# Optimization experiments

Hardware: AMD Instinct MI355X
Metric: run time of the kernel (lower is better)

Reference implementation:

```python
import jax, jax.numpy as jnp
import numpy as np

DIM = 384
NUM_HEADS = 6
HEAD_SIZE = DIM // NUM_HEADS


def setup_inputs() -> dict:
    key = jax.random.key(0)
    k1, k2, k3, k4, k5 = jax.random.split(key, 5)
    x = jax.random.normal(k1, (2, 4096, DIM), dtype=jnp.float32)
    # qkv Linear(dim, 3*dim): weight [3*dim, dim], bias [3*dim] (torch layout)
    w_qkv = jax.random.normal(k2, (3 * DIM, DIM), dtype=jnp.float32) * (1.0 / np.sqrt(DIM))
    b_qkv = jax.random.normal(k3, (3 * DIM,), dtype=jnp.float32) * 1e-6
    w_proj = jax.random.normal(k4, (DIM, DIM), dtype=jnp.float32) * (1.0 / np.sqrt(DIM))
    b_proj = jax.random.normal(k5, (DIM,), dtype=jnp.float32) * 0.01
    return {"x": x, "w_qkv": w_qkv, "b_qkv": b_qkv, "w_proj": w_proj, "b_proj": b_proj}


def reference(x, w_qkv, b_qkv, w_proj, b_proj):
    B, N, C = x.shape
    H, D = NUM_HEADS, HEAD_SIZE
    # qkv projection: [B, N, 3C]
    qkv = jnp.einsum("bnc,fc->bnf", x, w_qkv) + b_qkv
    # view(B, N, 3, H, D) -> permute to (3, B, H, N, D)
    qkv = qkv.reshape(B, N, 3, H, D).transpose(2, 0, 3, 1, 4)
    q, k, v = qkv[0], qkv[1], qkv[2]
    # full attention matrix [B, H, N, N] (matches the naive module)
    att = jnp.einsum("bhnd,bhmd->bhnm", q, k) / jnp.sqrt(jnp.float32(D)).astype(x.dtype)
    att = jax.nn.softmax(att, axis=-1)  # attn_drop p=0 -> identity
    out = jnp.einsum("bhnm,bhmd->bhnd", att, v)  # [B, H, N, D]
    out = out.transpose(0, 2, 1, 3).reshape(B, N, C)
    out = jnp.einsum("bnc,fc->bnf", out, w_proj) + b_proj  # proj_drop p=0 -> identity
    return out
```

## Files before the change

kernel.cpp:

```cpp
#include <hip/hip_runtime.h>
#include <stdint.h>

#define DIM   384
#define NH    6
#define SEQ   4096
#define MTOT  (2*SEQ)

typedef __bf16 bf16x8 __attribute__((ext_vector_type(8)));
typedef float  f32x4  __attribute__((ext_vector_type(4)));
typedef unsigned short u16;
typedef u16 u16x4 __attribute__((ext_vector_type(4)));
typedef u16 u16x8 __attribute__((ext_vector_type(8)));
typedef uint32_t u32x4 __attribute__((ext_vector_type(4)));

extern "C" __device__ float __ocml_native_exp2_f32(float);

__device__ __forceinline__ u16 f2b(float f) {
  uint32_t u = __builtin_bit_cast(uint32_t, f);
  u += 0x7fffu + ((u >> 16) & 1u);
  return (u16)(u >> 16);
}

#define GLDS16(gp, lp) \
  __builtin_amdgcn_global_load_lds((const __attribute__((address_space(1))) void*)(gp), \
                                   (__attribute__((address_space(3))) void*)(lp), 16, 0, 0)

__global__ void conv_bf16_kernel(const float* __restrict__ in, u16* __restrict__ out, int n8) {
  int i = blockIdx.x * 256 + threadIdx.x;
  if (i >= n8) return;
  float4 a = ((const float4*)in)[2*i];
  float4 b = ((const float4*)in)[2*i+1];
  u16x8 r;
  r[0]=f2b(a.x); r[1]=f2b(a.y); r[2]=f2b(a.z); r[3]=f2b(a.w);
  r[4]=f2b(b.x); r[5]=f2b(b.y); r[6]=f2b(b.z); r[7]=f2b(b.w);
  ((u16x8*)out)[i] = r;
}

template<int EPI>
__global__ __launch_bounds__(256) void gemm_bt_kernel(
    const u16* __restrict__ A,
    const u16* __restrict__ Bw,
    const float* __restrict__ bias,
    u16* __restrict__ Qb, u16* __restrict__ Kb, u16* __restrict__ Vt,
    float* __restrict__ Out)
{
  __shared__ u16 As[128*64];
  __shared__ u16 Bs[128*64];
  const int tid = threadIdx.x;
  const int wid = tid >> 6, lane = tid & 63;
  const int lr = lane & 15, lg = lane >> 4;
  const int m0 = blockIdx.x * 128;
  const int f0 = blockIdx.y * 128;
  const int wm = (wid >> 1) * 64, wn = (wid & 1) * 64;
  const f32x4 z4 = {0.f, 0.f, 0.f, 0.f};
  f32x4 acc[4][4];
  #pragma unroll
  for (int i = 0; i < 4; ++i)
    #pragma unroll
    for (int j = 0; j < 4; ++j) acc[i][j] = z4;

  for (int k0 = 0; k0 < 384; k0 += 64) {
    __syncthreads();
    #pragma unroll
    for (int i = 0; i < 4; ++i) {
      const int wb  = i*4096 + wid*1024;
      const int ob  = wb + lane*16;
      const int row = ob >> 7;
      const int lch = ((ob >> 4) & 7) ^ (row & 7);
      GLDS16(A  + (size_t)(m0+row)*384 + k0 + lch*8, As + wb/2);
      GLDS16(Bw + (size_t)(f0+row)*384 + k0 + lch*8, Bs + wb/2);
    }
    __syncthreads();
    #pragma unroll
    for (int ks = 0; ks < 2; ++ks) {
      bf16x8 af[4], bfr[4];
      #pragma unroll
      for (int mi = 0; mi < 4; ++mi) {
        int r = wm + mi*16 + lr;
        af[mi] = *(const bf16x8*)(As + (r*128 + ((ks*64 + lg*16) ^ ((r&7)<<4)))/2);
      }
      #pragma unroll
      for (int ni = 0; ni < 4; ++ni) {
        int r = wn + ni*16 + lr;
        bfr[ni] = *(const bf16x8*)(Bs + (r*128 + ((ks*64 + lg*16) ^ ((r&7)<<4)))/2);
      }
      #pragma unroll
      for (int mi = 0; mi < 4; ++mi)
        #pragma unroll
        for (int ni = 0; ni < 4; ++ni)
          acc[mi][ni] = __builtin_amdgcn_mfma_f32_16x16x32_bf16(af[mi], bfr[ni], acc[mi][ni], 0, 0, 0);
    }
  }

  if (EPI == 0) {
    const int which = f0 / 384;
    #pragma unroll
    for (int ni = 0; ni < 4; ++ni) {
      const int f   = f0 + wn + ni*16 + lr;
      const float bv = bias[f];
      const int rem = f - which*384;
      const int h = rem >> 6, d = rem & 63;
      #pragma unroll
      for (int mi = 0; mi < 4; ++mi) {
        const int m = m0 + wm + mi*16 + lg*4;
        const int b = m >> 12, n = m & 4095;
        const size_t bh = (size_t)(b*NH + h);
        if (which == 0) {
          #pragma unroll
          for (int j = 0; j < 4; ++j)
            Qb[(bh*SEQ + n + j)*64 + d] = f2b((acc[mi][ni][j] + bv) * 0.1803368801111244f);
        } else if (which == 1) {
          #pragma unroll
          for (int j = 0; j < 4; ++j)
            Kb[(bh*SEQ + n + j)*64 + d] = f2b(acc[mi][ni][j] + bv);
        } else {
          u16x4 pk;
          #pragma unroll
          for (int j = 0; j < 4; ++j) pk[j] = f2b(acc[mi][ni][j] + bv);
          *(u16x4*)(Vt + (bh*64 + d)*SEQ + n) = pk;
        }
      }
    }
  } else {
    #pragma unroll
    for (int ni = 0; ni < 4; ++ni) {
      const int f = f0 + wn + ni*16 + lr;
      const float bv = bias[f];
      #pragma unroll
      for (int mi = 0; mi < 4; ++mi) {
        const int m = m0 + wm + mi*16 + lg*4;
        #pragma unroll
        for (int j = 0; j < 4; ++j)
          Out[(size_t)(m+j)*DIM + f] = acc[mi][ni][j] + bv;
      }
    }
  }
}

__global__ __launch_bounds__(256, 3) void attn_kernel(
    const u16* __restrict__ Qb, const u16* __restrict__ Kb, const u16* __restrict__ Vt,
    u16* __restrict__ AO)
{
  __shared__ uint32_t smem[8192];
  char* sb = (char*)smem;
  const int tid = threadIdx.x;
  const int wid = tid >> 6, lane = tid & 63;
  const int lr = lane & 15, lg = lane >> 4;
  const int id = blockIdx.y * 64 + blockIdx.x;
  const int w  = (id & 7) * 96 + (id >> 3);
  const int bh = w >> 6;
  const int q0 = (w & 63) * 64;
  const u16* Qp = Qb + (size_t)bh*SEQ*64;
  const u16* Kp = Kb + (size_t)bh*SEQ*64;
  const u16* Vp = Vt + (size_t)bh*64*SEQ;

  bf16x8 qf[2];
  #pragma unroll
  for (int ks = 0; ks < 2; ++ks)
    qf[ks] = *(const bf16x8*)(Qp + (size_t)(q0 + wid*16 + lr)*64 + ks*32 + lg*8);

  bf16x8 onesf;
  {
    u32x4 ow = {0x3F803F80u, 0x3F803F80u, 0x3F803F80u, 0x3F803F80u};
    onesf = __builtin_bit_cast(bf16x8, ow);
  }

  const int la0 = lr*128 + ((lg*16) ^ ((lr&7)<<4));
  const int la1 = la0 ^ 64;

  const int r0  = tid >> 3;
  const int lch = (tid & 7) ^ (r0 & 7);
  const u16* kS  = Kp + r0*64 + lch*8;
  const u16* vS  = Vp + (size_t)r0*SEQ + lch*8;
  const u16* vS2 = Vp + (size_t)(r0+32)*SEQ + lch*8;
  char* kD = sb + tid*16;
  char* vD = sb + 16384 + tid*16;

  const f32x4 z4 = {0.f,0.f,0.f,0.f};
  f32x4 o[4] = {z4, z4, z4, z4};
  f32x4 ol = z4;
  f32x4 sA[4], sB[4];

  auto QK = [&](f32x4 (&s)[4], int KR) {
    __builtin_amdgcn_s_setprio(1);
    #pragma unroll
    for (int ni = 0; ni < 4; ++ni) {
      bf16x8 k0 = *(const bf16x8*)(sb + KR + ni*2048 + la0);
      bf16x8 k1 = *(const bf16x8*)(sb + KR + ni*2048 + la1);
      s[ni] = __builtin_amdgcn_mfma_f32_16x16x32_bf16(k0, qf[0], z4, 0, 0, 0);
      s[ni] = __builtin_amdgcn_mfma_f32_16x16x32_bf16(k1, qf[1], s[ni], 0, 0, 0);
    }
    __builtin_amdgcn_s_setprio(0);
  };

  auto SM_PV = [&](f32x4 (&s)[4], int VR) {
    #pragma unroll
    for (int ni = 0; ni < 4; ++ni)
      #pragma unroll
      for (int j = 0; j < 4; ++j)
        s[ni][j] = __ocml_native_exp2_f32(s[ni][j]);
    bf16x8 pf[2];
    #pragma unroll
    for (int ks = 0; ks < 2; ++ks) {
      uint32_t A, B, C, D;
      asm("v_cvt_pk_bf16_f32 %0, %1, %2" : "=v"(A) : "v"(s[2*ks][0]),   "v"(s[2*ks][1]));
      asm("v_cvt_pk_bf16_f32 %0, %1, %2" : "=v"(B) : "v"(s[2*ks][2]),   "v"(s[2*ks][3]));
      asm("v_cvt_pk_bf16_f32 %0, %1, %2" : "=v"(C) : "v"(s[2*ks+1][0]), "v"(s[2*ks+1][1]));
      asm("v_cvt_pk_bf16_f32 %0, %1, %2" : "=v"(D) : "v"(s[2*ks+1][2]), "v"(s[2*ks+1][3]));
      asm("v_permlane32_swap_b32 %0, %1" : "+v"(A), "+v"(C));
      asm("v_permlane16_swap_b32 %0, %1" : "+v"(A), "+v"(C));
      asm("v_permlane32_swap_b32 %0, %1" : "+v"(B), "+v"(D));
      asm("v_permlane16_swap_b32 %0, %1" : "+v"(B), "+v"(D));
      u32x4 wv = {A, B, C, D};
      pf[ks] = __builtin_bit_cast(bf16x8, wv);
    }
    __builtin_amdgcn_s_setprio(1);
    #pragma unroll
    for (int df = 0; df < 4; ++df) {
      bf16x8 v0 = *(const bf16x8*)(sb + 16384 + VR + df*2048 + la0);
      bf16x8 v1 = *(const bf16x8*)(sb + 16384 + VR + df*2048 + la1);
      o[df] = __builtin_amdgcn_mfma_f32_16x16x32_bf16(pf[0], v0, o[df], 0, 0, 0);
      o[df] = __builtin_amdgcn_mfma_f32_16x16x32_bf16(pf[1], v1, o[df], 0, 0, 0);
    }
    ol = __builtin_amdgcn_mfma_f32_16x16x32_bf16(pf[0], onesf, ol, 0, 0, 0);
    ol = __builtin_amdgcn_mfma_f32_16x16x32_bf16(pf[1], onesf, ol, 0, 0, 0);
    __builtin_amdgcn_s_setprio(0);
  };

  GLDS16(kS, kD);                 GLDS16(kS + 2048, kD + 4096);
  GLDS16(kS + 4096, kD + 8192);   GLDS16(kS + 4096 + 2048, kD + 8192 + 4096);
  GLDS16(vS, vD);                 GLDS16(vS2, vD + 4096);
  asm volatile("s_waitcnt vmcnt(0)" ::: "memory");
  __builtin_amdgcn_s_barrier();
  asm volatile("" ::: "memory");
  QK(sA, 0);
  __builtin_amdgcn_s_barrier();
  asm volatile("" ::: "memory");

  for (int t = 0; t < 62; t += 2) {
    GLDS16(kS + (t+2)*4096, kD);             GLDS16(kS + (t+2)*4096 + 2048, kD + 4096);
    GLDS16(vS + (t+1)*64, vD + 8192);        GLDS16(vS2 + (t+1)*64, vD + 8192 + 4096);
    QK(sB, 8192);
    SM_PV(sA, 0);
    asm volatile("s_waitcnt vmcnt(0)" ::: "memory");
    __builtin_amdgcn_s_barrier();
    asm volatile("" ::: "memory");
    GLDS16(kS + (t+3)*4096, kD + 8192);      GLDS16(kS + (t+3)*4096 + 2048, kD + 8192 + 4096);
    GLDS16(vS + (t+2)*64, vD);               GLDS16(vS2 + (t+2)*64, vD + 4096);
    QK(sA, 0);
    SM_PV(sB, 8192);
    asm volatile("s_waitcnt vmcnt(0)" ::: "memory");
    __builtin_amdgcn_s_barrier();
    asm volatile("" ::: "memory");
  }
  GLDS16(vS + 63*64, vD + 8192);             GLDS16(vS2 + 63*64, vD + 8192 + 4096);
  QK(sB, 8192);
  SM_PV(sA, 0);
  asm volatile("s_waitcnt vmcnt(0)" ::: "memory");
  __builtin_amdgcn_s_barrier();
  asm volatile("" ::: "memory");
  SM_PV(sB, 8192);

  const int b = bh / NH, h = bh - b*NH;
  float linv[4];
  #pragma unroll
  for (int j = 0; j < 4; ++j) linv[j] = 1.f / ol[j];
  #pragma unroll
  for (int df = 0; df < 4; ++df)
    #pragma unroll
    for (int j = 0; j < 4; ++j) {
      const int n = q0 + wid*16 + lg*4 + j;
      AO[((size_t)(b*SEQ + n))*DIM + h*64 + df*16 + lr] = f2b(o[df][j] * linv[j]);
    }
}

extern "C" void kernel_launch(void* const* d_in, const int* in_sizes, int n_in,
                              void* d_out, int out_size, void* d_ws, size_t ws_size,
                              hipStream_t stream) {
  const float* x      = (const float*)d_in[0];
  const float* w_qkv  = (const float*)d_in[1];
  const float* b_qkv  = (const float*)d_in[2];
  const float* w_proj = (const float*)d_in[3];
  const float* b_proj = (const float*)d_in[4];
  float* out = (float*)d_out;
  char* ws = (char*)d_ws;

  u16* xb  = (u16*)(ws);
  u16* wqb = (u16*)(ws + 6291456);
  u16* wpb = (u16*)(ws + 7176192);
  u16* Qb  = (u16*)(ws + 7471104);
  u16* Kb  = (u16*)(ws + 13762560);
  u16* Vt  = (u16*)(ws + 20054016);
  u16* AO  = (u16*)(ws + 26345472);

  {
    int n8 = (MTOT*DIM)/8;
    conv_bf16_kernel<<<dim3((n8+255)/256), dim3(256), 0, stream>>>(x, xb, n8);
  }
  {
    int n8 = (3*DIM*DIM)/8;
    conv_bf16_kernel<<<dim3((n8+255)/256), dim3(256), 0, stream>>>(w_qkv, wqb, n8);
  }
  {
    int n8 = (DIM*DIM)/8;
    conv_bf16_kernel<<<dim3((n8+255)/256), dim3(256), 0, stream>>>(w_proj, wpb, n8);
  }
  gemm_bt_kernel<0><<<dim3(MTOT/128, (3*DIM)/128), dim3(256), 0, stream>>>(
      xb, wqb, b_qkv, Qb, Kb, Vt, nullptr);
  attn_kernel<<<dim3(SEQ/64, 2*NH), dim3(256), 0, stream>>>(Qb, Kb, Vt, AO);
  gemm_bt_kernel<1><<<dim3(MTOT/128, DIM/128), dim3(256), 0, stream>>>(
      AO, wpb, b_proj, nullptr, nullptr, nullptr, out);
}
```

Measured before the change: 111.8 us.

## Double-buffer GEMM LDS staging and merge bf16 conversion launches

```diff
diff --git a/kernel.cpp b/kernel.cpp
--- a/kernel.cpp
+++ b/kernel.cpp
@@ -25,15 +25,20 @@
   __builtin_amdgcn_global_load_lds((const __attribute__((address_space(1))) void*)(gp), \
                                    (__attribute__((address_space(3))) void*)(lp), 16, 0, 0)
 
-__global__ void conv_bf16_kernel(const float* __restrict__ in, u16* __restrict__ out, int n8) {
+__global__ void conv_bf16_all(const float* __restrict__ x, const float* __restrict__ wq,
+                              const float* __restrict__ wp, u16* __restrict__ xb,
+                              u16* __restrict__ wqb, u16* __restrict__ wpb) {
   int i = blockIdx.x * 256 + threadIdx.x;
-  if (i >= n8) return;
-  float4 a = ((const float4*)in)[2*i];
-  float4 b = ((const float4*)in)[2*i+1];
+  const float* src; u16* dst; int off;
+  if (i < 393216)      { src = x;  dst = xb;  off = i; }
+  else if (i < 448512) { src = wq; dst = wqb; off = i - 393216; }
+  else                 { src = wp; dst = wpb; off = i - 448512; }
+  float4 a = ((const float4*)src)[2*off];
+  float4 b = ((const float4*)src)[2*off+1];
   u16x8 r;
   r[0]=f2b(a.x); r[1]=f2b(a.y); r[2]=f2b(a.z); r[3]=f2b(a.w);
   r[4]=f2b(b.x); r[5]=f2b(b.y); r[6]=f2b(b.z); r[7]=f2b(b.w);
-  ((u16x8*)out)[i] = r;
+  ((u16x8*)dst)[off] = r;
 }
 
 template<int EPI>
@@ -44,8 +49,8 @@
     u16* __restrict__ Qb, u16* __restrict__ Kb, u16* __restrict__ Vt,
     float* __restrict__ Out)
 {
-  __shared__ u16 As[128*64];
-  __shared__ u16 Bs[128*64];
+  __shared__ u16 As[2][128*64];
+  __shared__ u16 Bs[2][128*64];
   const int tid = threadIdx.x;
   const int wid = tid >> 6, lane = tid & 63;
   const int lr = lane & 15, lg = lane >> 4;
@@ -59,30 +64,43 @@
     #pragma unroll
     for (int j = 0; j < 4; ++j) acc[i][j] = z4;
 
-  for (int k0 = 0; k0 < 384; k0 += 64) {
-    __syncthreads();
+  auto stage = [&](int k, int buf) {
+    const int k0 = k * 64;
     #pragma unroll
     for (int i = 0; i < 4; ++i) {
       const int wb  = i*4096 + wid*1024;
       const int ob  = wb + lane*16;
       const int row = ob >> 7;
       const int lch = ((ob >> 4) & 7) ^ (row & 7);
-      GLDS16(A  + (size_t)(m0+row)*384 + k0 + lch*8, As + wb/2);
-      GLDS16(Bw + (size_t)(f0+row)*384 + k0 + lch*8, Bs + wb/2);
-    }
-    __syncthreads();
+      GLDS16(A  + (size_t)(m0+row)*384 + k0 + lch*8, &As[buf][0] + wb/2);
+      GLDS16(Bw + (size_t)(f0+row)*384 + k0 + lch*8, &Bs[buf][0] + wb/2);
+    }
+  };
+
+  stage(0, 0);
+  #pragma unroll
+  for (int k = 0; k < 6; ++k) {
+    const int cur = k & 1;
+    if (k < 5) {
+      stage(k+1, cur ^ 1);
+      asm volatile("s_waitcnt vmcnt(8)" ::: "memory");
+    } else {
+      asm volatile("s_waitcnt vmcnt(0)" ::: "memory");
+    }
+    __builtin_amdgcn_s_barrier();
+    asm volatile("" ::: "memory");
     #pragma unroll
     for (int ks = 0; ks < 2; ++ks) {
       bf16x8 af[4], bfr[4];
       #pragma unroll
       for (int mi = 0; mi < 4; ++mi) {
         int r = wm + mi*16 + lr;
-        af[mi] = *(const bf16x8*)(As + (r*128 + ((ks*64 + lg*16) ^ ((r&7)<<4)))/2);
+        af[mi] = *(const bf16x8*)(&As[cur][0] + (r*128 + ((ks*64 + lg*16) ^ ((r&7)<<4)))/2);
       }
       #pragma unroll
       for (int ni = 0; ni < 4; ++ni) {
         int r = wn + ni*16 + lr;
-        bfr[ni] = *(const bf16x8*)(Bs + (r*128 + ((ks*64 + lg*16) ^ ((r&7)<<4)))/2);
+        bfr[ni] = *(const bf16x8*)(&Bs[cur][0] + (r*128 + ((ks*64 + lg*16) ^ ((r&7)<<4)))/2);
       }
       #pragma unroll
       for (int mi = 0; mi < 4; ++mi)
@@ -90,6 +108,8 @@
         for (int ni = 0; ni < 4; ++ni)
           acc[mi][ni] = __builtin_amdgcn_mfma_f32_16x16x32_bf16(af[mi], bfr[ni], acc[mi][ni], 0, 0, 0);
     }
+    __builtin_amdgcn_s_barrier();
+    asm volatile("" ::: "memory");
   }
 
   if (EPI == 0) {
@@ -293,18 +313,7 @@
   u16* Vt  = (u16*)(ws + 20054016);
   u16* AO  = (u16*)(ws + 26345472);
 
-  {
-    int n8 = (MTOT*DIM)/8;
-    conv_bf16_kernel<<<dim3((n8+255)/256), dim3(256), 0, stream>>>(x, xb, n8);
-  }
-  {
-    int n8 = (3*DIM*DIM)/8;
-    conv_bf16_kernel<<<dim3((n8+255)/256), dim3(256), 0, stream>>>(w_qkv, wqb, n8);
-  }
-  {
-    int n8 = (DIM*DIM)/8;
-    conv_bf16_kernel<<<dim3((n8+255)/256), dim3(256), 0, stream>>>(w_proj, wpb, n8);
-  }
+  conv_bf16_all<<<dim3(1824), dim3(256), 0, stream>>>(x, w_qkv, w_proj, xb, wqb, wpb);
   gemm_bt_kernel<0><<<dim3(MTOT/128, (3*DIM)/128), dim3(256), 0, stream>>>(
       xb, wqb, b_qkv, Qb, Kb, Vt, nullptr);
   attn_kernel<<<dim3(SEQ/64, 2*NH), dim3(256), 0, stream>>>(Qb, Kb, Vt, AO);
```

Result: faster. 101.8 us (-9.0%).
